# Kernel optimization log

Measured on AMD Instinct MI355X. Metric: run time of the kernel, lower is better.

## Reference

```python
import math
import jax, jax.numpy as jnp
import numpy as np

N_EMBD = 1024
N_HEAD = 16
HEAD_DIM = N_EMBD // N_HEAD


def setup_inputs() -> dict:
    key = jax.random.key(0)
    k1, k2, k3, k4, k5 = jax.random.split(key, 5)
    B, T, C = 1, 4096, N_EMBD
    s = 1.0 / math.sqrt(C)
    return {
        "x": jax.random.normal(k1, (B, T, C), dtype=jnp.float32),
        "w_qkv": jax.random.normal(k2, (C, 3 * C), dtype=jnp.float32) * s,
        "b_qkv": jnp.zeros((3 * C,), dtype=jnp.float32),
        "w_proj": jax.random.normal(k3, (C, C), dtype=jnp.float32) * s,
        "b_proj": jnp.zeros((C,), dtype=jnp.float32),
    }


def reference(x, w_qkv, b_qkv, w_proj, b_proj):
    B, T, C = x.shape
    qkv = x @ w_qkv + b_qkv                       # [B,T,3C]
    q, k, v = jnp.split(qkv, 3, axis=-1)
    # [B,T,C] -> [B,H,T,D]
    def heads(t):
        return t.reshape(B, T, N_HEAD, HEAD_DIM).transpose(0, 2, 1, 3)
    q, k, v = heads(q), heads(k), heads(v)
    scale = 1.0 / math.sqrt(HEAD_DIM)
    attn = jnp.einsum("bhqd,bhkd->bhqk", q, k) * scale
    causal = jnp.tril(jnp.ones((T, T), dtype=bool))
    attn = jnp.where(causal, attn, -jnp.inf)
    attn = jax.nn.softmax(attn, axis=-1)
    out = jnp.einsum("bhqk,bhkd->bhqd", attn, v)   # [B,H,T,D]
    out = out.transpose(0, 2, 1, 3).reshape(B, T, C)
    return out @ w_proj + b_proj
```

## Files before the change

### kernel.cpp

```cpp
#include <hip/hip_runtime.h>
#include <hip/hip_bf16.h>

#define TT 4096
#define CC 1024
#define NHEAD 16
#define DH 64
#define N3C 3072

typedef __attribute__((ext_vector_type(8))) short short8;
typedef __attribute__((ext_vector_type(4))) float floatx4;

#define QSCALE 0.18033688011112042f

__device__ __forceinline__ short f2bf(float f) {
    union { __hip_bfloat16 h; short s; } u;
    u.h = __float2bfloat16(f);
    return u.s;
}

__device__ __forceinline__ void gload_lds16(const void* g, void* l) {
    __builtin_amdgcn_global_load_lds(
        (const __attribute__((address_space(1))) unsigned int*)(unsigned long long)g,
        (__attribute__((address_space(3))) unsigned int*)(unsigned int)(unsigned long long)l,
        16, 0, 0);
}

__device__ __forceinline__ unsigned pk_trunc(float lo, float hi) {
    return __builtin_amdgcn_perm(__float_as_uint(hi), __float_as_uint(lo), 0x07060302u);
}

__device__ __forceinline__ void tr_body(const float* __restrict__ in, short* __restrict__ out,
                                        int K, int N, int bx, int by, int tid, float (*tile)[33]) {
    int nt = bx * 32, kt = by * 32;
    int tx = tid & 31, ty = tid >> 5;
#pragma unroll
    for (int i = 0; i < 32; i += 8)
        tile[ty + i][tx] = in[(size_t)(kt + ty + i) * N + nt + tx];
    __syncthreads();
#pragma unroll
    for (int i = 0; i < 32; i += 8)
        out[(size_t)(nt + ty + i) * K + kt + tx] = f2bf(tile[tx][ty + i]);
}

__global__ void k_prep(const float* __restrict__ x, short* __restrict__ xb,
                       const float* __restrict__ w_qkv, short* __restrict__ wqkvT,
                       const float* __restrict__ w_proj, short* __restrict__ wprojT) {
    __shared__ float tile[32][33];
    int id = blockIdx.x;
    int tid = threadIdx.x;
    if (id < 4096) {
        int i = (id * 256 + tid) * 4;
        float4 v = *(const float4*)&x[i];
        short4 r;
        r.x = f2bf(v.x); r.y = f2bf(v.y); r.z = f2bf(v.z); r.w = f2bf(v.w);
        *(short4*)&xb[i] = r;
    } else if (id < 4096 + 3072) {
        int r = id - 4096;
        tr_body(w_qkv, wqkvT, CC, N3C, r % 96, r / 96, tid, tile);
    } else {
        int r = id - 7168;
        tr_body(w_proj, wprojT, CC, CC, r & 31, r >> 5, tid, tile);
    }
}

__global__ __launch_bounds__(256) void k_gemm_qkv(const short* __restrict__ A,
                                                  const short* __restrict__ Bt,
                                                  const float* __restrict__ bias,
                                                  short* __restrict__ Q,
                                                  short* __restrict__ Kb,
                                                  short* __restrict__ Vtg) {
    const int m0 = blockIdx.y * 128;
    const int n0 = blockIdx.x * 128;
    __shared__ __attribute__((aligned(16))) short As[2][128 * 32];
    __shared__ __attribute__((aligned(16))) short Bs[2][128 * 32];
    const int tid = threadIdx.x;
    const int lane = tid & 63;
    const int w = tid >> 6;
    const int wm = w >> 1, wn = w & 1;
    const int quad = lane >> 4;
    const int l16 = lane & 15;

    const int r0 = tid >> 2, c0 = (tid & 3) * 8;
    const short* pA[2][2]; const short* pB[2][2];
    short* lA[2][2]; short* lB[2][2];
#pragma unroll
    for (int it = 0; it < 2; ++it)
#pragma unroll
        for (int hh = 0; hh < 2; ++hh) {
            pA[it][hh] = A + (size_t)(m0 + it * 64 + r0) * CC + hh * 32 + c0;
            pB[it][hh] = Bt + (size_t)(n0 + it * 64 + r0) * CC + hh * 32 + c0;
            lA[it][hh] = &As[hh][(it * 256 + w * 64) * 8];
            lB[it][hh] = &Bs[hh][(it * 256 + w * 64) * 8];
        }

    floatx4 acc[4][4] = {};
    for (int kb = 0; kb < CC; kb += 64) {
        __syncthreads();
#pragma unroll
        for (int it = 0; it < 2; ++it)
#pragma unroll
            for (int hh = 0; hh < 2; ++hh) {
                gload_lds16(pA[it][hh] + kb, lA[it][hh]);
                gload_lds16(pB[it][hh] + kb, lB[it][hh]);
            }
        __syncthreads();
#pragma unroll
        for (int kk = 0; kk < 2; ++kk) {
            short8 af[4], bf[4];
#pragma unroll
            for (int mi = 0; mi < 4; ++mi)
                af[mi] = *(const short8*)&As[kk][(wm * 64 + mi * 16 + l16) * 32 + quad * 8];
#pragma unroll
            for (int ni = 0; ni < 4; ++ni)
                bf[ni] = *(const short8*)&Bs[kk][(wn * 64 + ni * 16 + l16) * 32 + quad * 8];
#pragma unroll
            for (int mi = 0; mi < 4; ++mi)
#pragma unroll
                for (int ni = 0; ni < 4; ++ni)
                    acc[mi][ni] = __builtin_amdgcn_mfma_f32_16x16x32_bf16(af[mi], bf[ni], acc[mi][ni], 0, 0, 0);
        }
    }
#pragma unroll
    for (int mi = 0; mi < 4; ++mi) {
#pragma unroll
        for (int ni = 0; ni < 4; ++ni) {
            int gm = m0 + wm * 64 + mi * 16 + quad * 4;
            int gn = n0 + wn * 64 + ni * 16 + l16;
            int which = gn >> 10;
            int cc = gn & 1023;
            int h = cc >> 6, d = cc & 63;
            float bv = bias[gn];
            if (which == 0) {
#pragma unroll
                for (int r = 0; r < 4; ++r) {
                    float v = (acc[mi][ni][r] + bv) * QSCALE;
                    Q[((size_t)h * TT + (gm + r)) * DH + d] = f2bf(v);
                }
            } else if (which == 1) {
#pragma unroll
                for (int r = 0; r < 4; ++r) {
                    float v = acc[mi][ni][r] + bv;
                    Kb[((size_t)h * TT + (gm + r)) * DH + d] = f2bf(v);
                }
            } else {
                short4 vv;
                vv.x = f2bf(acc[mi][ni][0] + bv);
                vv.y = f2bf(acc[mi][ni][1] + bv);
                vv.z = f2bf(acc[mi][ni][2] + bv);
                vv.w = f2bf(acc[mi][ni][3] + bv);
                *(short4*)&Vtg[((size_t)h * DH + d) * TT + gm] = vv;
            }
        }
    }
}

__global__ __launch_bounds__(256) void k_attn(const short* __restrict__ Qh,
                                              const short* __restrict__ Kh,
                                              const short* __restrict__ VhT,
                                              short* __restrict__ Ob) {
    const int h = blockIdx.x;
    const int pair = blockIdx.y;
    const int tid = threadIdx.x, lane = tid & 63, w = tid >> 6;
    const int quad = lane >> 4, l16 = lane & 15;

    __shared__ __attribute__((aligned(16))) short Ps[2][64 * 136];
    __shared__ float wl[4][64];
    __shared__ float lsum[64];

    const short* Qp = Qh + (size_t)h * TT * DH;
    const short* Kp = Kh + (size_t)h * TT * DH;
    const short* Vp = VhT + (size_t)h * DH * TT;

    int buf = 0;

#pragma unroll 1
    for (int half = 0; half < 2; ++half) {
        const int qi = half ? (63 - pair) : pair;
        const int q0 = qi * 64;
        const int nk = (qi >> 1) + 1;

        short8 aq[4][2];
#pragma unroll
        for (int qg = 0; qg < 4; ++qg)
#pragma unroll
            for (int s = 0; s < 2; ++s)
                aq[qg][s] = *(const short8*)&Qp[(size_t)(q0 + qg * 16 + l16) * DH + s * 32 + quad * 8];

        floatx4 accO[4] = {};
        float l_part[4] = {0.f, 0.f, 0.f, 0.f};

        for (int ki = 0; ki < nk; ++ki) {
            const int k0 = ki * 128;
            const bool masked = (ki == nk - 1);

            short8 kf[2][2];
#pragma unroll
            for (int mi = 0; mi < 2; ++mi)
#pragma unroll
                for (int s = 0; s < 2; ++s)
                    kf[mi][s] = *(const short8*)&Kp[(size_t)(k0 + w * 32 + mi * 16 + l16) * DH + s * 32 + quad * 8];

            floatx4 accS[2][4] = {};
#pragma unroll
            for (int mi = 0; mi < 2; ++mi)
#pragma unroll
                for (int s = 0; s < 2; ++s)
#pragma unroll
                    for (int qg = 0; qg < 4; ++qg)
                        accS[mi][qg] = __builtin_amdgcn_mfma_f32_16x16x32_bf16(kf[mi][s], aq[qg][s], accS[mi][qg], 0, 0, 0);

            short* Pb = &Ps[buf][0];
#pragma unroll
            for (int mi = 0; mi < 2; ++mi) {
                const int kbase = k0 + w * 32 + mi * 16 + quad * 4;
#pragma unroll
                for (int qg = 0; qg < 4; ++qg) {
                    float p[4];
#pragma unroll
                    for (int r = 0; r < 4; ++r) {
                        float e = __builtin_amdgcn_exp2f(accS[mi][qg][r]);
                        if (masked)
                            e = (kbase + r <= q0 + qg * 16 + l16) ? e : 0.f;
                        p[r] = e;
                        l_part[qg] += e;
                    }
                    uint2 pk;
                    pk.x = pk_trunc(p[0], p[1]);
                    pk.y = pk_trunc(p[2], p[3]);
                    *(uint2*)&Pb[(qg * 16 + l16) * 136 + w * 32 + mi * 16 + quad * 4] = pk;
                }
            }

            short8 vf[4];
#pragma unroll
            for (int ks = 0; ks < 4; ++ks)
                vf[ks] = *(const short8*)&Vp[(size_t)(w * 16 + l16) * TT + k0 + ks * 32 + quad * 8];

            __syncthreads();

#pragma unroll
            for (int qg = 0; qg < 4; ++qg)
#pragma unroll
                for (int ks = 0; ks < 4; ++ks) {
                    short8 ap = *(const short8*)&Pb[(qg * 16 + l16) * 136 + ks * 32 + quad * 8];
                    accO[qg] = __builtin_amdgcn_mfma_f32_16x16x32_bf16(ap, vf[ks], accO[qg], 0, 0, 0);
                }
            buf ^= 1;
        }

#pragma unroll
        for (int qg = 0; qg < 4; ++qg) {
            float lr = l_part[qg];
            lr += __shfl_xor(lr, 16, 64);
            lr += __shfl_xor(lr, 32, 64);
            if (lane < 16) wl[w][qg * 16 + lane] = lr;
        }
        __syncthreads();
        if (tid < 64) lsum[tid] = wl[0][tid] + wl[1][tid] + wl[2][tid] + wl[3][tid];
        __syncthreads();

#pragma unroll
        for (int qg = 0; qg < 4; ++qg) {
#pragma unroll
            for (int r = 0; r < 4; ++r) {
                int q = qg * 16 + quad * 4 + r;
                float o = accO[qg][r] / lsum[q];
                Ob[(size_t)(q0 + q) * CC + h * DH + w * 16 + l16] = f2bf(o);
            }
        }
    }
}

__global__ __launch_bounds__(256) void k_gemm_proj(const short* __restrict__ A,
                                                   const short* __restrict__ Bt,
                                                   const float* __restrict__ bias,
                                                   float* __restrict__ out) {
    const int m0 = blockIdx.y * 128;
    const int n0 = blockIdx.x * 128;
    __shared__ __attribute__((aligned(16))) short As[2][128 * 32];
    __shared__ __attribute__((aligned(16))) short Bs[2][128 * 32];
    const int tid = threadIdx.x;
    const int lane = tid & 63;
    const int w = tid >> 6;
    const int wm = w >> 1, wn = w & 1;
    const int quad = lane >> 4;
    const int l16 = lane & 15;

    const int r0 = tid >> 2, c0 = (tid & 3) * 8;
    const short* pA[2][2]; const short* pB[2][2];
    short* lA[2][2]; short* lB[2][2];
#pragma unroll
    for (int it = 0; it < 2; ++it)
#pragma unroll
        for (int hh = 0; hh < 2; ++hh) {
            pA[it][hh] = A + (size_t)(m0 + it * 64 + r0) * CC + hh * 32 + c0;
            pB[it][hh] = Bt + (size_t)(n0 + it * 64 + r0) * CC + hh * 32 + c0;
            lA[it][hh] = &As[hh][(it * 256 + w * 64) * 8];
            lB[it][hh] = &Bs[hh][(it * 256 + w * 64) * 8];
        }

    floatx4 acc[4][4] = {};
    for (int kb = 0; kb < CC; kb += 64) {
        __syncthreads();
#pragma unroll
        for (int it = 0; it < 2; ++it)
#pragma unroll
            for (int hh = 0; hh < 2; ++hh) {
                gload_lds16(pA[it][hh] + kb, lA[it][hh]);
                gload_lds16(pB[it][hh] + kb, lB[it][hh]);
            }
        __syncthreads();
#pragma unroll
        for (int kk = 0; kk < 2; ++kk) {
            short8 af[4], bf[4];
#pragma unroll
            for (int mi = 0; mi < 4; ++mi)
                af[mi] = *(const short8*)&As[kk][(wm * 64 + mi * 16 + l16) * 32 + quad * 8];
#pragma unroll
            for (int ni = 0; ni < 4; ++ni)
                bf[ni] = *(const short8*)&Bs[kk][(wn * 64 + ni * 16 + l16) * 32 + quad * 8];
#pragma unroll
            for (int mi = 0; mi < 4; ++mi)
#pragma unroll
                for (int ni = 0; ni < 4; ++ni)
                    acc[mi][ni] = __builtin_amdgcn_mfma_f32_16x16x32_bf16(af[mi], bf[ni], acc[mi][ni], 0, 0, 0);
        }
    }
#pragma unroll
    for (int mi = 0; mi < 4; ++mi) {
#pragma unroll
        for (int ni = 0; ni < 4; ++ni) {
            int gm = m0 + wm * 64 + mi * 16 + quad * 4;
            int gn = n0 + wn * 64 + ni * 16 + l16;
            float bv = bias[gn];
#pragma unroll
            for (int r = 0; r < 4; ++r)
                out[(size_t)(gm + r) * CC + gn] = acc[mi][ni][r] + bv;
        }
    }
}

extern "C" void kernel_launch(void* const* d_in, const int* in_sizes, int n_in,
                              void* d_out, int out_size, void* d_ws, size_t ws_size,
                              hipStream_t stream) {
    const float* x      = (const float*)d_in[0];
    const float* w_qkv  = (const float*)d_in[1];
    const float* b_qkv  = (const float*)d_in[2];
    const float* w_proj = (const float*)d_in[3];
    const float* b_proj = (const float*)d_in[4];
    float* out = (float*)d_out;
    char* ws = (char*)d_ws;

    short* xb     = (short*)(ws);
    short* wqkvT  = (short*)(ws + 8388608);
    short* wprojT = (short*)(ws + 14680064);
    short* Qh     = (short*)(ws + 16777216);
    short* Kh     = (short*)(ws + 25165824);
    short* VhT    = (short*)(ws + 33554432);
    short* Ob     = (short*)(ws + 41943040);

    k_prep<<<8192, 256, 0, stream>>>(x, xb, w_qkv, wqkvT, w_proj, wprojT);
    k_gemm_qkv<<<dim3(N3C / 128, TT / 128), 256, 0, stream>>>(xb, wqkvT, b_qkv, Qh, Kh, VhT);
    k_attn<<<dim3(NHEAD, 32), 256, 0, stream>>>(Qh, Kh, VhT, Ob);
    k_gemm_proj<<<dim3(CC / 128, TT / 128), 256, 0, stream>>>(Ob, wprojT, b_proj, out);
}
```

Baseline: 216.0 us.

## Split attention key range across waves with per-wave P buffers and final reduction

```diff
diff --git a/kernel.cpp b/kernel.cpp
--- a/kernel.cpp
+++ b/kernel.cpp
@@ -154,30 +154,38 @@
     }
 }
 
-__global__ __launch_bounds__(256) void k_attn(const short* __restrict__ Qh,
-                                              const short* __restrict__ Kh,
-                                              const short* __restrict__ VhT,
-                                              short* __restrict__ Ob) {
+__global__ __launch_bounds__(256, 2) void k_attn(const short* __restrict__ Qh,
+                                                 const short* __restrict__ Kh,
+                                                 const short* __restrict__ VhT,
+                                                 short* __restrict__ Ob) {
     const int h = blockIdx.x;
     const int pair = blockIdx.y;
     const int tid = threadIdx.x, lane = tid & 63, w = tid >> 6;
     const int quad = lane >> 4, l16 = lane & 15;
 
-    __shared__ __attribute__((aligned(16))) short Ps[2][64 * 136];
-    __shared__ float wl[4][64];
-    __shared__ float lsum[64];
+    __shared__ __attribute__((aligned(16))) short Pws[4][2048];
+    __shared__ __attribute__((aligned(16))) float Red[4][2][5][256];
 
     const short* Qp = Qh + (size_t)h * TT * DH;
     const short* Kp = Kh + (size_t)h * TT * DH;
     const short* Vp = VhT + (size_t)h * DH * TT;
-
-    int buf = 0;
+    short* Pw = &Pws[w][0];
+
+    const int wslot = quad * 16 + ((l16 + quad * 4) & 15);
+    const int qcA = (quad & 1) * 2, qcB = qcA + 1;
+    const int rslotA = qcA * 16 + ((l16 + qcA * 4) & 15);
+    const int rslotB = qcB * 16 + ((l16 + qcB * 4) & 15);
+    const int mi_r = quad >> 1;
+
+    short8 onesB;
+#pragma unroll
+    for (int j = 0; j < 8; ++j) onesB[j] = (short)0x3F80;
 
 #pragma unroll 1
     for (int half = 0; half < 2; ++half) {
         const int qi = half ? (63 - pair) : pair;
         const int q0 = qi * 64;
-        const int nk = (qi >> 1) + 1;
+        const int qmax = q0 + 63;
 
         short8 aq[4][2];
 #pragma unroll
@@ -186,19 +194,20 @@
             for (int s = 0; s < 2; ++s)
                 aq[qg][s] = *(const short8*)&Qp[(size_t)(q0 + qg * 16 + l16) * DH + s * 32 + quad * 8];
 
-        floatx4 accO[4] = {};
-        float l_part[4] = {0.f, 0.f, 0.f, 0.f};
-
-        for (int ki = 0; ki < nk; ++ki) {
-            const int k0 = ki * 128;
-            const bool masked = (ki == nk - 1);
-
+        floatx4 accO[4][4] = {};
+        floatx4 accL[4] = {};
+
+        auto strip = [&](int k0, bool masked) {
+            short8 vf[4];
+#pragma unroll
+            for (int dg = 0; dg < 4; ++dg)
+                vf[dg] = *(const short8*)&Vp[(size_t)(dg * 16 + l16) * TT + k0 + quad * 8];
             short8 kf[2][2];
 #pragma unroll
             for (int mi = 0; mi < 2; ++mi)
 #pragma unroll
                 for (int s = 0; s < 2; ++s)
-                    kf[mi][s] = *(const short8*)&Kp[(size_t)(k0 + w * 32 + mi * 16 + l16) * DH + s * 32 + quad * 8];
+                    kf[mi][s] = *(const short8*)&Kp[(size_t)(k0 + mi * 16 + l16) * DH + s * 32 + quad * 8];
 
             floatx4 accS[2][4] = {};
 #pragma unroll
@@ -209,10 +218,9 @@
                     for (int qg = 0; qg < 4; ++qg)
                         accS[mi][qg] = __builtin_amdgcn_mfma_f32_16x16x32_bf16(kf[mi][s], aq[qg][s], accS[mi][qg], 0, 0, 0);
 
-            short* Pb = &Ps[buf][0];
+            const int kq = k0 - q0 + quad * 4;
 #pragma unroll
             for (int mi = 0; mi < 2; ++mi) {
-                const int kbase = k0 + w * 32 + mi * 16 + quad * 4;
 #pragma unroll
                 for (int qg = 0; qg < 4; ++qg) {
                     float p[4];
@@ -220,52 +228,62 @@
                     for (int r = 0; r < 4; ++r) {
                         float e = __builtin_amdgcn_exp2f(accS[mi][qg][r]);
                         if (masked)
-                            e = (kbase + r <= q0 + qg * 16 + l16) ? e : 0.f;
+                            e = (kq + mi * 16 + r <= qg * 16 + l16) ? e : 0.f;
                         p[r] = e;
-                        l_part[qg] += e;
                     }
                     uint2 pk;
                     pk.x = pk_trunc(p[0], p[1]);
                     pk.y = pk_trunc(p[2], p[3]);
-                    *(uint2*)&Pb[(qg * 16 + l16) * 136 + w * 32 + mi * 16 + quad * 4] = pk;
-                }
-            }
-
-            short8 vf[4];
-#pragma unroll
-            for (int ks = 0; ks < 4; ++ks)
-                vf[ks] = *(const short8*)&Vp[(size_t)(w * 16 + l16) * TT + k0 + ks * 32 + quad * 8];
-
+                    *(uint2*)&Pw[((mi * 4 + qg) * 64 + wslot) * 4] = pk;
+                }
+            }
+#pragma unroll
+            for (int qg = 0; qg < 4; ++qg) {
+                const int blk = (mi_r * 4 + qg) * 64;
+                union { uint4 u; short8 s; } af;
+                *(uint2*)&af.u.x = *(const uint2*)&Pw[(blk + rslotA) * 4];
+                *(uint2*)&af.u.z = *(const uint2*)&Pw[(blk + rslotB) * 4];
+#pragma unroll
+                for (int dg = 0; dg < 4; ++dg)
+                    accO[qg][dg] = __builtin_amdgcn_mfma_f32_16x16x32_bf16(af.s, vf[dg], accO[qg][dg], 0, 0, 0);
+                accL[qg] = __builtin_amdgcn_mfma_f32_16x16x32_bf16(af.s, onesB, accL[qg], 0, 0, 0);
+            }
+        };
+
+        int tmp = q0 - 32 - w * 32;
+        int nfull = (tmp >= 0) ? ((tmp >> 7) + 1) : 0;
+        for (int c = 0; c < nfull; ++c) strip(c * 128 + w * 32, false);
+        int k0d = nfull * 128 + w * 32;
+        if (k0d <= qmax) strip(k0d, true);
+
+#pragma unroll 1
+        for (int ph = 0; ph < 2; ++ph) {
             __syncthreads();
-
-#pragma unroll
-            for (int qg = 0; qg < 4; ++qg)
-#pragma unroll
-                for (int ks = 0; ks < 4; ++ks) {
-                    short8 ap = *(const short8*)&Pb[(qg * 16 + l16) * 136 + ks * 32 + quad * 8];
-                    accO[qg] = __builtin_amdgcn_mfma_f32_16x16x32_bf16(ap, vf[ks], accO[qg], 0, 0, 0);
-                }
-            buf ^= 1;
-        }
-
-#pragma unroll
-        for (int qg = 0; qg < 4; ++qg) {
-            float lr = l_part[qg];
-            lr += __shfl_xor(lr, 16, 64);
-            lr += __shfl_xor(lr, 32, 64);
-            if (lane < 16) wl[w][qg * 16 + lane] = lr;
-        }
-        __syncthreads();
-        if (tid < 64) lsum[tid] = wl[0][tid] + wl[1][tid] + wl[2][tid] + wl[3][tid];
-        __syncthreads();
-
-#pragma unroll
-        for (int qg = 0; qg < 4; ++qg) {
-#pragma unroll
-            for (int r = 0; r < 4; ++r) {
-                int q = qg * 16 + quad * 4 + r;
-                float o = accO[qg][r] / lsum[q];
-                Ob[(size_t)(q0 + q) * CC + h * DH + w * 16 + l16] = f2bf(o);
+#pragma unroll
+            for (int g = 0; g < 2; ++g) {
+                int qg = ph * 2 + g;
+#pragma unroll
+                for (int dg = 0; dg < 4; ++dg)
+                    *(floatx4*)&Red[w][g][dg][lane * 4] = accO[qg][dg];
+                *(floatx4*)&Red[w][g][4][lane * 4] = accL[qg];
+            }
+            __syncthreads();
+#pragma unroll
+            for (int g = 0; g < 2; ++g) {
+                int qg = ph * 2 + g;
+                floatx4 os = {}, ls = {};
+#pragma unroll
+                for (int sw = 0; sw < 4; ++sw) {
+                    floatx4 o = *(const floatx4*)&Red[sw][g][w][lane * 4];
+                    floatx4 l = *(const floatx4*)&Red[sw][g][4][lane * 4];
+                    os += o; ls += l;
+                }
+#pragma unroll
+                for (int r = 0; r < 4; ++r) {
+                    int q = qg * 16 + quad * 4 + r;
+                    float o = os[r] / ls[r];
+                    Ob[(size_t)(q0 + q) * CC + h * DH + w * 16 + l16] = f2bf(o);
+                }
             }
         }
     }
```

New measurement: 237.9 us. +10.2%, slower.
